# Optimization experiments

Measured on AMD Instinct MI355X. Metric: run time of the kernel, lower is better.

Reference implementation:

```python
import jax, jax.numpy as jnp
import numpy as np

SIGMA_AGG = 0.5
SIGMA_DIS = 3.0
ALPHA = 0.5
BETA = 0.25
EPS = 1e-5
K_MAX = 8  # number of kernel/text instances per image; labels in {0..K_MAX}, 0 = background


def setup_inputs() -> dict:
    key = jax.random.key(0)
    ks = jax.random.split(key, 7)
    B, C, H, W = 16, 4, 640, 640
    return dict(
        pred_regions=jax.random.normal(ks[0], (B, 1, H, W), jnp.float32),
        regions_gt=jax.random.randint(ks[1], (B, 1, H, W), 0, 2).astype(jnp.float32),
        pred_kernels=jax.random.normal(ks[2], (B, 1, H, W), jnp.float32),
        kernels_gt=jax.random.randint(ks[3], (B, 1, H, W), 0, 2).astype(jnp.float32),
        pred_similarities=jax.random.normal(ks[4], (B, C, H, W), jnp.float32),
        text_mask_ndi_labels=jax.random.randint(ks[5], (B, H, W), 0, K_MAX + 1, dtype=jnp.int32),
        kernel_mask_ndi_labels=jax.random.randint(ks[6], (B, H, W), 0, K_MAX + 1, dtype=jnp.int32),
    )


def _dice_loss(pred, gt, eps):
    # sigmoid -> per-sample dice, summed over batch (matches Text/KernelDiceLoss)
    p = jax.nn.sigmoid(pred).reshape(pred.shape[0], -1)
    g = gt.reshape(gt.shape[0], -1)
    inter = jnp.sum(p * g, axis=1)
    denom = (jnp.sum(p * p, axis=1) + eps) + (jnp.sum(g * g, axis=1) + eps)
    dice = (2.0 * inter + eps) / denom
    return jnp.sum(1.0 - dice)


def _agg_dis_single(sim, tlab, klab):
    # sim: (C, H, W); tlab/klab: (H, W) int instance labels (0 = background)
    C = sim.shape[0]
    sim = sim.reshape(C, -1)
    tlab = tlab.reshape(-1)
    klab = klab.reshape(-1)
    nseg = K_MAX + 1

    s2 = jnp.sum(sim * sim, axis=0)  # per-pixel squared feature norm, (N,)
    ones = jnp.ones_like(s2)
    ck = jax.ops.segment_sum(ones, klab, num_segments=nseg)  # kernel cardinalities
    ct = jax.ops.segment_sum(ones, tlab, num_segments=nseg)  # text cardinalities

    # Aggregation: || sim*1[T==i] - sim*1[K==i]/(ck_i+1) ||_F per instance i.
    # Per pixel, nonzero only for i = tlab[p] or i = klab[p]:
    inv = 1.0 / (ck + 1.0)
    same = tlab == klab
    coef_t = jnp.where(same, (1.0 - inv[klab]) ** 2, 1.0)  # contributes to instance tlab
    coef_k = jnp.where(same, 0.0, inv[klab] ** 2)          # contributes to instance klab
    n2 = (jax.ops.segment_sum(s2 * coef_t, tlab, num_segments=nseg)
          + jax.ops.segment_sum(s2 * coef_k, klab, num_segments=nseg))
    norm = jnp.sqrt(n2[1:])  # drop background segment 0
    # NOTE: torch.max(scalar, 0)[0] on a 0-d tensor is identity (no clamp) - reproduced here.
    l_agg = jnp.sum(jnp.log((norm - SIGMA_AGG) ** 2 + 1.0) / (ct[1:] + 1.0))

    # Discrimination: kernel masks are disjoint, so
    # ||mu_i - mu_j||_F^2 = a_i + a_j with a_i = sum_{K==i} s2 / (ck_i + 0.001)^2
    a = jax.ops.segment_sum(s2, klab, num_segments=nseg)[1:] / (ck[1:] + 0.001) ** 2
    pair = SIGMA_DIS - jnp.sqrt(a[:, None] + a[None, :])
    val = jnp.log(pair ** 2 + 1.0)
    triu = jnp.triu(jnp.ones((K_MAX, K_MAX), bool), 1)
    l_dis = jnp.sum(jnp.where(triu, val, 0.0)) / (K_MAX * (K_MAX - 1))
    return l_agg, l_dis


def reference(pred_regions, regions_gt, pred_kernels, kernels_gt,
              pred_similarities, text_mask_ndi_labels, kernel_mask_ndi_labels):
    # OHEM mask is computed in the torch code but never used by TextDiceLoss, so it is omitted.
    loss_regions = _dice_loss(pred_regions, regions_gt, EPS)
    loss_kernel = _dice_loss(pred_kernels, kernels_gt, EPS)
    l_agg, l_dis = jax.vmap(_agg_dis_single)(pred_similarities,
                                             text_mask_ndi_labels,
                                             kernel_mask_ndi_labels)
    loss_aggregation = jnp.sum(l_agg)
    loss_discrimination = jnp.sum(l_dis)
    loss = loss_regions + ALPHA * loss_kernel + BETA * (loss_aggregation + loss_discrimination)
    return (loss, loss_regions, loss_kernel, loss_aggregation, loss_discrimination)
```

## Files before the change

kernel.cpp:

```cpp
#include <hip/hip_runtime.h>
#include <math.h>


#define NSEG 9
#define NACC 51
#define NBATCH 16
#define EPSF 1e-5f
#define GX 100
#define NITER 4

__device__ __forceinline__ float wave_reduce_sum(float v) {
#pragma unroll
    for (int off = 32; off > 0; off >>= 1)
        v += __shfl_down(v, off, 64);
    return v;
}

__device__ __forceinline__ float sigm(float x) {
    return 1.0f / (1.0f + __expf(-x));
}

__global__ __launch_bounds__(256, 4) void pan_main(
    const float* __restrict__ pred_r, const float* __restrict__ gt_r,
    const float* __restrict__ pred_k, const float* __restrict__ gt_k,
    const float* __restrict__ sim,
    const int* __restrict__ tlab, const int* __restrict__ klab,
    float* __restrict__ ws, int npix)
{
    const int tid = threadIdx.x;
    const int b = blockIdx.y;
    const long long base = (long long)b * npix;
    const long long sbase = (long long)b * 4 * npix;

    const float4* pr4 = (const float4*)(pred_r + base);
    const float4* gr4 = (const float4*)(gt_r + base);
    const float4* pk4 = (const float4*)(pred_k + base);
    const float4* gk4 = (const float4*)(gt_k + base);
    const float4* c0_4 = (const float4*)(sim + sbase);
    const float4* c1_4 = (const float4*)(sim + sbase + npix);
    const float4* c2_4 = (const float4*)(sim + sbase + 2LL * npix);
    const float4* c3_4 = (const float4*)(sim + sbase + 3LL * npix);
    const int4* tl4 = (const int4*)(tlab + base);
    const int4* kl4 = (const int4*)(klab + base);

    float St_[8], Sk_[8], Ss_[8];
    unsigned ct_[8], ck_[8];
#pragma unroll
    for (int s = 0; s < 8; ++s) {
        St_[s] = 0.0f; Sk_[s] = 0.0f; Ss_[s] = 0.0f;
        ct_[s] = 0u; ck_[s] = 0u;
    }
    float rpg = 0.0f, rpp = 0.0f, rgg = 0.0f;
    float kpg = 0.0f, kpp = 0.0f, kgg = 0.0f;

    int i = blockIdx.x * blockDim.x + tid;
    const int stride = GX * 256;

    float4 pr = pr4[i], gr = gr4[i], pk = pk4[i], gk = gk4[i];
    float4 c0 = c0_4[i], c1 = c1_4[i], c2 = c2_4[i], c3 = c3_4[i];
    int4 tl = tl4[i], kl = kl4[i];

#pragma unroll
    for (int t = 0; t < NITER; ++t) {
        float4 n_pr, n_gr, n_pk, n_gk, n_c0, n_c1, n_c2, n_c3;
        int4 n_tl, n_kl;
        if (t + 1 < NITER) {
            const int j = i + stride;
            n_pr = pr4[j]; n_gr = gr4[j]; n_pk = pk4[j]; n_gk = gk4[j];
            n_c0 = c0_4[j]; n_c1 = c1_4[j]; n_c2 = c2_4[j]; n_c3 = c3_4[j];
            n_tl = tl4[j]; n_kl = kl4[j];
        }

        {
            float p;
            p = sigm(pr.x); rpg += p * gr.x; rpp += p * p; rgg += gr.x;
            p = sigm(pr.y); rpg += p * gr.y; rpp += p * p; rgg += gr.y;
            p = sigm(pr.z); rpg += p * gr.z; rpp += p * p; rgg += gr.z;
            p = sigm(pr.w); rpg += p * gr.w; rpp += p * p; rgg += gr.w;
            p = sigm(pk.x); kpg += p * gk.x; kpp += p * p; kgg += gk.x;
            p = sigm(pk.y); kpg += p * gk.y; kpp += p * p; kgg += gk.y;
            p = sigm(pk.z); kpg += p * gk.z; kpp += p * p; kgg += gk.z;
            p = sigm(pk.w); kpg += p * gk.w; kpp += p * p; kgg += gk.w;
        }

        float s2x = c0.x * c0.x + c1.x * c1.x + c2.x * c2.x + c3.x * c3.x;
        float s2y = c0.y * c0.y + c1.y * c1.y + c2.y * c2.y + c3.y * c3.y;
        float s2z = c0.z * c0.z + c1.z * c1.z + c2.z * c2.z + c3.z * c3.z;
        float s2w = c0.w * c0.w + c1.w * c1.w + c2.w * c2.w + c3.w * c3.w;

#define DO_COMP(TL, KL, S2)                                          \
        {                                                            \
            bool tt = ((TL) == s);                                   \
            bool kk = ((KL) == s);                                   \
            ct_[s - 1] += (unsigned)__popcll(__ballot(tt));          \
            ck_[s - 1] += (unsigned)__popcll(__ballot(kk));          \
            St_[s - 1] += tt ? (S2) : 0.0f;                          \
            Sk_[s - 1] += kk ? (S2) : 0.0f;                          \
            Ss_[s - 1] += (tt && kk) ? (S2) : 0.0f;                  \
        }

#pragma unroll
        for (int s = 1; s <= 8; ++s) {
            DO_COMP(tl.x, kl.x, s2x);
            DO_COMP(tl.y, kl.y, s2y);
            DO_COMP(tl.z, kl.z, s2z);
            DO_COMP(tl.w, kl.w, s2w);
        }
#undef DO_COMP

        if (t + 1 < NITER) {
            pr = n_pr; gr = n_gr; pk = n_pk; gk = n_gk;
            c0 = n_c0; c1 = n_c1; c2 = n_c2; c3 = n_c3;
            tl = n_tl; kl = n_kl;
            i += stride;
        }
    }

    __shared__ float red[4][NACC];
    const int lane = tid & 63;
    const int wv = tid >> 6;

#pragma unroll
    for (int s = 0; s < 8; ++s) {
        float v;
        v = wave_reduce_sum(St_[s]); if (lane == 0) red[wv][19 + s] = v;
        v = wave_reduce_sum(Sk_[s]); if (lane == 0) red[wv][28 + s] = v;
        v = wave_reduce_sum(Ss_[s]); if (lane == 0) red[wv][37 + s] = v;
    }
    {
        float v;
        v = wave_reduce_sum(rpg); if (lane == 0) red[wv][45] = v;
        v = wave_reduce_sum(rpp); if (lane == 0) red[wv][46] = v;
        v = wave_reduce_sum(rgg); if (lane == 0) red[wv][47] = v;
        v = wave_reduce_sum(kpg); if (lane == 0) red[wv][48] = v;
        v = wave_reduce_sum(kpp); if (lane == 0) red[wv][49] = v;
        v = wave_reduce_sum(kgg); if (lane == 0) red[wv][50] = v;
    }
    if (lane == 0) {
#pragma unroll
        for (int s = 0; s < 8; ++s) {
            red[wv][1 + s] = (float)ct_[s];
            red[wv][10 + s] = (float)ck_[s];
        }
        red[wv][0] = 0.0f; red[wv][9] = 0.0f; red[wv][18] = 0.0f;
        red[wv][27] = 0.0f; red[wv][36] = 0.0f;
    }
    __syncthreads();
    if (tid < NACC) {
        float s = red[0][tid] + red[1][tid] + red[2][tid] + red[3][tid];
        atomicAdd(&ws[b * NACC + tid], s);
    }
}

__global__ __launch_bounds__(64) void pan_finalize(
    const float* __restrict__ ws, float* __restrict__ out)
{
    const int b = threadIdx.x;
    float dice_r = 0.0f, dice_k = 0.0f, lagg = 0.0f, ldis = 0.0f;

    if (b < NBATCH) {
        const float* w = ws + b * NACC;
        {
            float pg = w[45], pp = w[46], gg = w[47];
            dice_r = 1.0f - (2.0f * pg + EPSF) / ((pp + EPSF) + (gg + EPSF));
            pg = w[48]; pp = w[49]; gg = w[50];
            dice_k = 1.0f - (2.0f * pg + EPSF) / ((pp + EPSF) + (gg + EPSF));
        }
        float a[8];
#pragma unroll
        for (int i = 1; i < NSEG; ++i) {
            float ct = w[i], ck = w[NSEG + i];
            float St = w[2 * NSEG + i], Sk = w[3 * NSEG + i], Ss = w[4 * NSEG + i];
            float inv = 1.0f / (ck + 1.0f);
            float omi = 1.0f - inv;
            float n2 = omi * omi * Ss + (St - Ss) + inv * inv * (Sk - Ss);
            float nrm = sqrtf(n2);
            float d = nrm - 0.5f;
            lagg += logf(d * d + 1.0f) / (ct + 1.0f);
            float ckd = ck + 0.001f;
            a[i - 1] = Sk / (ckd * ckd);
        }
#pragma unroll
        for (int i = 0; i < 8; ++i) {
#pragma unroll
            for (int j = i + 1; j < 8; ++j) {
                float pair = 3.0f - sqrtf(a[i] + a[j]);
                ldis += logf(pair * pair + 1.0f);
            }
        }
        ldis *= (1.0f / 56.0f);
    }

    dice_r = wave_reduce_sum(dice_r);
    dice_k = wave_reduce_sum(dice_k);
    lagg = wave_reduce_sum(lagg);
    ldis = wave_reduce_sum(ldis);

    if (threadIdx.x == 0) {
        float loss = dice_r + 0.5f * dice_k + 0.25f * (lagg + ldis);
        out[0] = loss;
        out[1] = dice_r;
        out[2] = dice_k;
        out[3] = lagg;
        out[4] = ldis;
    }
}

extern "C" void kernel_launch(void* const* d_in, const int* in_sizes, int n_in,
                              void* d_out, int out_size, void* d_ws, size_t ws_size,
                              hipStream_t stream) {
    const float* pred_r = (const float*)d_in[0];
    const float* gt_r   = (const float*)d_in[1];
    const float* pred_k = (const float*)d_in[2];
    const float* gt_k   = (const float*)d_in[3];
    const float* sim    = (const float*)d_in[4];
    const int*   tlab   = (const int*)d_in[5];
    const int*   klab   = (const int*)d_in[6];
    float* out = (float*)d_out;
    float* ws  = (float*)d_ws;

    const int npix = in_sizes[0] / NBATCH;

    hipMemsetAsync(ws, 0, NBATCH * NACC * sizeof(float), stream);

    dim3 grid(GX, NBATCH);
    pan_main<<<grid, 256, 0, stream>>>(pred_r, gt_r, pred_k, gt_k, sim,
                                       tlab, klab, ws, npix);
    pan_finalize<<<1, 64, 0, stream>>>(ws, out);
}
```

Before: 296.4 us.

## Stage inputs through LDS with async global_load_lds and halve grid

Replaces the register-prefetched float4 global loads with __builtin_amdgcn_global_load_lds copies of 16 bytes per lane into a 40KB shared buffer, followed by a barrier and LDS reads. The grid shrinks from 100 to 50 blocks per image, and each block now handles 8 tiles instead of 4 strided ones. The aim is to cut VGPR pressure and issue DMA-style loads directly into LDS. However, there is no double buffering, so each tile waits on its own loads and then pays two barriers. The 40KB of LDS per block also limits occupancy.

```diff
diff --git a/kernel.cpp b/kernel.cpp
--- a/kernel.cpp
+++ b/kernel.cpp
@@ -6,8 +6,8 @@
 #define NACC 51
 #define NBATCH 16
 #define EPSF 1e-5f
-#define GX 100
-#define NITER 4
+#define BPB 50
+#define TPB 8
 
 __device__ __forceinline__ float wave_reduce_sum(float v) {
 #pragma unroll
@@ -19,6 +19,11 @@
 __device__ __forceinline__ float sigm(float x) {
     return 1.0f / (1.0f + __expf(-x));
 }
+
+#define ASYNC16(G, L)                                                        \
+    __builtin_amdgcn_global_load_lds(                                        \
+        (const __attribute__((address_space(1))) void*)(G),                  \
+        (__attribute__((address_space(3))) void*)(L), 16, 0, 0)
 
 __global__ __launch_bounds__(256, 4) void pan_main(
     const float* __restrict__ pred_r, const float* __restrict__ gt_r,
@@ -27,21 +32,26 @@
     const int* __restrict__ tlab, const int* __restrict__ klab,
     float* __restrict__ ws, int npix)
 {
+    __shared__ float lds[10 * 1024];
+
     const int tid = threadIdx.x;
     const int b = blockIdx.y;
     const long long base = (long long)b * npix;
     const long long sbase = (long long)b * 4 * npix;
 
-    const float4* pr4 = (const float4*)(pred_r + base);
-    const float4* gr4 = (const float4*)(gt_r + base);
-    const float4* pk4 = (const float4*)(pred_k + base);
-    const float4* gk4 = (const float4*)(gt_k + base);
-    const float4* c0_4 = (const float4*)(sim + sbase);
-    const float4* c1_4 = (const float4*)(sim + sbase + npix);
-    const float4* c2_4 = (const float4*)(sim + sbase + 2LL * npix);
-    const float4* c3_4 = (const float4*)(sim + sbase + 3LL * npix);
-    const int4* tl4 = (const int4*)(tlab + base);
-    const int4* kl4 = (const int4*)(klab + base);
+    const char* p0 = (const char*)(pred_r + base);
+    const char* p1 = (const char*)(gt_r + base);
+    const char* p2 = (const char*)(pred_k + base);
+    const char* p3 = (const char*)(gt_k + base);
+    const char* p4 = (const char*)(sim + sbase);
+    const char* p5 = (const char*)(sim + sbase + npix);
+    const char* p6 = (const char*)(sim + sbase + 2LL * npix);
+    const char* p7 = (const char*)(sim + sbase + 3LL * npix);
+    const char* p8 = (const char*)(tlab + base);
+    const char* p9 = (const char*)(klab + base);
+
+    char* lbase = (char*)lds;
+    const unsigned woff = (unsigned)(tid & ~63) * 16;
 
     float St_[8], Sk_[8], Ss_[8];
     unsigned ct_[8], ck_[8];
@@ -53,23 +63,33 @@
     float rpg = 0.0f, rpp = 0.0f, rgg = 0.0f;
     float kpg = 0.0f, kpp = 0.0f, kgg = 0.0f;
 
-    int i = blockIdx.x * blockDim.x + tid;
-    const int stride = GX * 256;
-
-    float4 pr = pr4[i], gr = gr4[i], pk = pk4[i], gk = gk4[i];
-    float4 c0 = c0_4[i], c1 = c1_4[i], c2 = c2_4[i], c3 = c3_4[i];
-    int4 tl = tl4[i], kl = kl4[i];
-
-#pragma unroll
-    for (int t = 0; t < NITER; ++t) {
-        float4 n_pr, n_gr, n_pk, n_gk, n_c0, n_c1, n_c2, n_c3;
-        int4 n_tl, n_kl;
-        if (t + 1 < NITER) {
-            const int j = i + stride;
-            n_pr = pr4[j]; n_gr = gr4[j]; n_pk = pk4[j]; n_gk = gk4[j];
-            n_c0 = c0_4[j]; n_c1 = c1_4[j]; n_c2 = c2_4[j]; n_c3 = c3_4[j];
-            n_tl = tl4[j]; n_kl = kl4[j];
-        }
+    for (int t = 0; t < TPB; ++t) {
+        const long long g16 = ((long long)(blockIdx.x * TPB + t) * 256 + tid) * 16;
+
+        ASYNC16(p0 + g16, lbase + 0 * 4096 + woff);
+        ASYNC16(p1 + g16, lbase + 1 * 4096 + woff);
+        ASYNC16(p2 + g16, lbase + 2 * 4096 + woff);
+        ASYNC16(p3 + g16, lbase + 3 * 4096 + woff);
+        ASYNC16(p4 + g16, lbase + 4 * 4096 + woff);
+        ASYNC16(p5 + g16, lbase + 5 * 4096 + woff);
+        ASYNC16(p6 + g16, lbase + 6 * 4096 + woff);
+        ASYNC16(p7 + g16, lbase + 7 * 4096 + woff);
+        ASYNC16(p8 + g16, lbase + 8 * 4096 + woff);
+        ASYNC16(p9 + g16, lbase + 9 * 4096 + woff);
+
+        __syncthreads();
+
+        const int toff = tid * 16;
+        const float4 pr = *(const float4*)(lbase + 0 * 4096 + toff);
+        const float4 gr = *(const float4*)(lbase + 1 * 4096 + toff);
+        const float4 pk = *(const float4*)(lbase + 2 * 4096 + toff);
+        const float4 gk = *(const float4*)(lbase + 3 * 4096 + toff);
+        const float4 c0 = *(const float4*)(lbase + 4 * 4096 + toff);
+        const float4 c1 = *(const float4*)(lbase + 5 * 4096 + toff);
+        const float4 c2 = *(const float4*)(lbase + 6 * 4096 + toff);
+        const float4 c3 = *(const float4*)(lbase + 7 * 4096 + toff);
+        const int4 tl = *(const int4*)(lbase + 8 * 4096 + toff);
+        const int4 kl = *(const int4*)(lbase + 9 * 4096 + toff);
 
         {
             float p;
@@ -83,10 +103,10 @@
             p = sigm(pk.w); kpg += p * gk.w; kpp += p * p; kgg += gk.w;
         }
 
-        float s2x = c0.x * c0.x + c1.x * c1.x + c2.x * c2.x + c3.x * c3.x;
-        float s2y = c0.y * c0.y + c1.y * c1.y + c2.y * c2.y + c3.y * c3.y;
-        float s2z = c0.z * c0.z + c1.z * c1.z + c2.z * c2.z + c3.z * c3.z;
-        float s2w = c0.w * c0.w + c1.w * c1.w + c2.w * c2.w + c3.w * c3.w;
+        const float s2x = c0.x * c0.x + c1.x * c1.x + c2.x * c2.x + c3.x * c3.x;
+        const float s2y = c0.y * c0.y + c1.y * c1.y + c2.y * c2.y + c3.y * c3.y;
+        const float s2z = c0.z * c0.z + c1.z * c1.z + c2.z * c2.z + c3.z * c3.z;
+        const float s2w = c0.w * c0.w + c1.w * c1.w + c2.w * c2.w + c3.w * c3.w;
 
 #define DO_COMP(TL, KL, S2)                                          \
         {                                                            \
@@ -108,12 +128,7 @@
         }
 #undef DO_COMP
 
-        if (t + 1 < NITER) {
-            pr = n_pr; gr = n_gr; pk = n_pk; gk = n_gk;
-            c0 = n_c0; c1 = n_c1; c2 = n_c2; c3 = n_c3;
-            tl = n_tl; kl = n_kl;
-            i += stride;
-        }
+        __syncthreads();
     }
 
     __shared__ float red[4][NACC];
@@ -223,7 +238,7 @@
 
     hipMemsetAsync(ws, 0, NBATCH * NACC * sizeof(float), stream);
 
-    dim3 grid(GX, NBATCH);
+    dim3 grid(BPB, NBATCH);
     pan_main<<<grid, 256, 0, stream>>>(pred_r, gt_r, pred_k, gt_k, sim,
                                        tlab, klab, ws, npix);
     pan_finalize<<<1, 64, 0, stream>>>(ws, out);
```

After: 296.6 us. Within noise of the previous version (+0.1%).
